# Performance work log

Measured on AMD Instinct MI355X. Metric: run time of the kernel, lower is better.

The kernel has to match this reference:

```python
import jax, jax.numpy as jnp
import numpy as np

INPUT_DIM = 1024
OUTPUT_DIM = 1024
NUM_HEADS = 16  # NOTE: torch .split(num_heads) => chunk SIZE = num_heads
N_CHUNKS = OUTPUT_DIM // NUM_HEADS  # 64 effective heads of dim 16
NEG_INF = -1e9


def setup_inputs() -> dict:
    key = jax.random.key(0)
    k1, k2, k3, k4 = jax.random.split(key, 4)
    B, S = 32, 256
    x = jax.random.normal(k1, (B, S, INPUT_DIM), dtype=jnp.float32)
    mask = jnp.ones((B, S), dtype=jnp.float32)
    # xavier-uniform-ish linear weights, torch layout [out, in]
    lim = float(np.sqrt(6.0 / (INPUT_DIM + OUTPUT_DIM)))
    Wq = jax.random.uniform(k2, (OUTPUT_DIM, INPUT_DIM), jnp.float32, -lim, lim)
    Wk = jax.random.uniform(k3, (OUTPUT_DIM, INPUT_DIM), jnp.float32, -lim, lim)
    Wv = jax.random.uniform(k4, (OUTPUT_DIM, INPUT_DIM), jnp.float32, -lim, lim)
    return {"batch_sequence": x, "sequence_mask": mask, "Wq": Wq, "Wk": Wk, "Wv": Wv}


def _split_heads(m):
    # [B,S,D] -> chunks of size NUM_HEADS stacked in dim 0: [C,B,S,H]
    B, S, D = m.shape
    return jnp.transpose(m.reshape(B, S, N_CHUNKS, NUM_HEADS), (2, 0, 1, 3))


def reference(batch_sequence, sequence_mask, Wq, Wk, Wv):
    q = _split_heads(batch_sequence @ Wq.T)  # [C,B,S,H]
    k = _split_heads(batch_sequence @ Wk.T)
    v = _split_heads(batch_sequence @ Wv.T)
    logits = jnp.einsum("cbqh,cbkh->cbqk", q, k) / jnp.sqrt(
        jnp.asarray(OUTPUT_DIM, batch_sequence.dtype)
    )
    mask2d = sequence_mask[:, :, None] * sequence_mask[:, None, :]  # [B,S,S]
    logits = jnp.where(mask2d[None] > 0, logits, NEG_INF)
    w = jax.nn.softmax(logits, axis=-1)
    out = jnp.einsum("cbqk,cbkh->cbqh", w, v)  # [C,B,S,H]
    B, S = batch_sequence.shape[:2]
    return jnp.transpose(out, (1, 2, 0, 3)).reshape(B, S, OUTPUT_DIM)
```

## Files before the change

### kernel.cpp

```cpp
#include <hip/hip_runtime.h>


typedef unsigned short u16;
typedef unsigned int u32;
typedef __attribute__((ext_vector_type(8))) short short8;
typedef __attribute__((ext_vector_type(4))) short short4v;
typedef __attribute__((ext_vector_type(4))) float floatx4;

#if __has_builtin(__builtin_amdgcn_mfma_f32_16x16x16bf16_1k)
#define MFMA16(A, B, C) __builtin_amdgcn_mfma_f32_16x16x16bf16_1k(A, B, C, 0, 0, 0)
#elif __has_builtin(__builtin_amdgcn_mfma_f32_16x16x16_bf16)
#define MFMA16(A, B, C) __builtin_amdgcn_mfma_f32_16x16x16_bf16(A, B, C, 0, 0, 0)
#else
__device__ __forceinline__ floatx4 mfma16_asm(short4v a, short4v b, floatx4 c) {
  floatx4 d;
  asm volatile("v_mfma_f32_16x16x16_bf16 %0, %1, %2, %3"
               : "=v"(d) : "v"(a), "v"(b), "v"(c));
  return d;
}
#define MFMA16(A, B, C) mfma16_asm(A, B, C)
#endif

#if __has_builtin(__builtin_amdgcn_exp2f)
#define EXP2(x) __builtin_amdgcn_exp2f(x)
#else
#define EXP2(x) __expf((x) * 0.6931471805599453f)
#endif

#define QSCALE 0.045084220f

__device__ __forceinline__ u16 f2bf(float f) {
  union { float f; u32 u; } x; x.f = f;
  u32 r = x.u + 0x7fffu + ((x.u >> 16) & 1u);
  return (u16)(r >> 16);
}
__device__ __forceinline__ float bf2f(u16 u) {
  union { u32 u; float f; } x; x.u = ((u32)u) << 16;
  return x.f;
}

__device__ __forceinline__ void gload16(const void* g, void* l) {
  typedef __attribute__((address_space(1))) const unsigned int gq;
  typedef __attribute__((address_space(3))) unsigned int lq;
  __builtin_amdgcn_global_load_lds((gq*)(size_t)g, (lq*)(size_t)l, 16, 0, 0);
}

#define GK 1024
#define QKS 20
#define VTS 264

__global__ __launch_bounds__(256) void cast_all(const float* __restrict__ x,
                                                const float* __restrict__ wq,
                                                const float* __restrict__ wk,
                                                const float* __restrict__ wv,
                                                u16* __restrict__ XB,
                                                u16* __restrict__ WB) {
  int bid = blockIdx.x;
  const float* src; u16* dst; int off;
  if (bid < 8192)       { src = x;  dst = XB;                 off = bid; }
  else if (bid < 9216)  { src = wq; dst = WB;                 off = bid - 8192; }
  else if (bid < 10240) { src = wk; dst = WB + 1024 * 1024;   off = bid - 9216; }
  else                  { src = wv; dst = WB + 2 * 1024 * 1024; off = bid - 10240; }
  int i = (off * 256 + threadIdx.x) * 4;
  float4 v = *(const float4*)(src + i);
  u32 lo = (u32)f2bf(v.x) | ((u32)f2bf(v.y) << 16);
  u32 hi = (u32)f2bf(v.z) | ((u32)f2bf(v.w) << 16);
  uint2 o; o.x = lo; o.y = hi;
  *(uint2*)(dst + i) = o;
}

template <bool MASKED>
__device__ __forceinline__ void attn_loop2(const u16* __restrict__ Ks,
                                           const u16* __restrict__ Vt,
                                           const short4v* bq, const float* mqv,
                                           const float* m_s,
                                           floatx4* oacc, floatx4* lacc,
                                           int col, int quad) {
  const short4v ones = {(short)0x3F80, (short)0x3F80, (short)0x3F80, (short)0x3F80};
#pragma unroll 4
  for (int kt = 0; kt < 16; kt++) {
    const int kb = kt * 16;
    short4v ak = *(const short4v*)(Ks + (kb + col) * QKS + quad * 4);
    short4v av = *(const short4v*)(Vt + col * VTS + kb + quad * 4);
    float mk[4];
    if (MASKED) {
#pragma unroll
      for (int i = 0; i < 4; i++) mk[i] = m_s[kb + quad * 4 + i];
    }
#pragma unroll
    for (int qt = 0; qt < 2; qt++) {
      floatx4 z = {0.f, 0.f, 0.f, 0.f};
      floatx4 st = MFMA16(ak, bq[qt], z);
      float e[4];
#pragma unroll
      for (int i = 0; i < 4; i++) {
        e[i] = EXP2(st[i]);
        if (MASKED) e[i] = (mqv[qt] * mk[i] > 0.f) ? e[i] : 0.f;
      }
      union { u32 u[2]; short4v s; } pk;
      pk.u[0] = __builtin_amdgcn_perm(__float_as_uint(e[1]), __float_as_uint(e[0]), 0x07060302u);
      pk.u[1] = __builtin_amdgcn_perm(__float_as_uint(e[3]), __float_as_uint(e[2]), 0x07060302u);
      lacc[qt] = MFMA16(ones, pk.s, lacc[qt]);
      oacc[qt] = MFMA16(av, pk.s, oacc[qt]);
    }
  }
}

__global__ __launch_bounds__(512, 4) void fused_qkv_attn(const u16* __restrict__ XB,
                                                         const u16* __restrict__ WB,
                                                         const float* __restrict__ mask,
                                                         float* __restrict__ out) {
  __shared__ __align__(16) u16 smem[22528];
  __shared__ float m_s[256];

  const int bid = blockIdx.x;
  const int b = bid & 31;
  const int c0 = (bid >> 5) * 2;
  const int t = threadIdx.x;
  const int wave = t >> 6;
  const int lane = t & 63;
  const int col = lane & 15;
  const int quad = lane >> 4;

  u16* const Xs = smem;
  u16* const Ws = smem + 16384;

  float mv = (t < 256) ? mask[b * 256 + t] : 1.0f;
  if (t < 256) m_s[t] = mv;
  const int allones = __syncthreads_and(mv > 0.f);

  const int r_loc = lane >> 3;
  const int sch = (lane & 7) ^ r_loc;

  const size_t xsrc = ((size_t)b * 256 + wave * 32 + r_loc) * GK + sch * 8;
  const int xdst = wave * 2048;

  const int gA = wave;
  const int ntA = gA >> 1;
  const size_t wsrcA =
      ((size_t)((ntA % 3) * 1024 + (c0 + ntA / 3) * 16 + (gA & 1) * 8 + r_loc)) * GK + sch * 8;
  size_t wsrcB = 0;
  const int gB = 8 + wave;
  if (wave < 4) {
    const int ntB = gB >> 1;
    wsrcB = ((size_t)((ntB % 3) * 1024 + (c0 + ntB / 3) * 16 + (gB & 1) * 8 + r_loc)) * GK + sch * 8;
  }

  floatx4 acc[2][6] = {};

  for (int k0 = 0; k0 < GK; k0 += 64) {
    __syncthreads();
#pragma unroll
    for (int g = 0; g < 4; g++)
      gload16(XB + xsrc + (size_t)g * 8 * GK + k0, Xs + xdst + g * 512);
    gload16(WB + wsrcA + k0, Ws + gA * 512);
    if (wave < 4) gload16(WB + wsrcB + k0, Ws + gB * 512);
    __syncthreads();
#pragma unroll
    for (int kk = 0; kk < 2; kk++) {
      const int pos = ((kk * 4 + quad) ^ (col & 7)) * 8;
      short8 af[2], bf[6];
#pragma unroll
      for (int mt = 0; mt < 2; mt++)
        af[mt] = *(const short8*)(Xs + (wave * 32 + mt * 16 + col) * 64 + pos);
#pragma unroll
      for (int nt = 0; nt < 6; nt++)
        bf[nt] = *(const short8*)(Ws + (nt * 16 + col) * 64 + pos);
#pragma unroll
      for (int mt = 0; mt < 2; mt++)
#pragma unroll
        for (int nt = 0; nt < 6; nt++)
          acc[mt][nt] = __builtin_amdgcn_mfma_f32_16x16x32_bf16(af[mt], bf[nt], acc[mt][nt], 0, 0, 0);
    }
  }

  u16* const Qs = smem;
  u16* const Ks = smem + 5120;
  u16* const Vt = smem + 10240;
  float* const l_s = (float*)(smem + 14464);
  float* const ot = (float*)smem;

#pragma unroll
  for (int h = 0; h < 2; h++) {
    __syncthreads();

#pragma unroll
    for (int mt = 0; mt < 2; mt++) {
      const int row = wave * 32 + mt * 16 + quad * 4;
#pragma unroll
      for (int r = 0; r < 4; r++) {
        Qs[(row + r) * QKS + col] = f2bf(acc[mt][3 * h + 0][r] * QSCALE);
        Ks[(row + r) * QKS + col] = f2bf(acc[mt][3 * h + 1][r]);
        Vt[col * VTS + row + r] = f2bf(acc[mt][3 * h + 2][r]);
      }
    }
    __syncthreads();

    const int q0 = wave * 32;
    short4v bq[2];
    float mqv[2];
#pragma unroll
    for (int qt = 0; qt < 2; qt++) {
      bq[qt] = *(const short4v*)(Qs + (q0 + qt * 16 + col) * QKS + quad * 4);
      mqv[qt] = m_s[q0 + qt * 16 + col];
    }

    floatx4 oacc[2] = {};
    floatx4 lacc[2] = {};
    if (allones)
      attn_loop2<false>(Ks, Vt, bq, mqv, m_s, oacc, lacc, col, quad);
    else
      attn_loop2<true>(Ks, Vt, bq, mqv, m_s, oacc, lacc, col, quad);

    __syncthreads();
#pragma unroll
    for (int qt = 0; qt < 2; qt++) {
      if (quad == 0) l_s[q0 + qt * 16 + col] = lacc[qt][0];
#pragma unroll
      for (int r = 0; r < 4; r++)
        ot[(quad * 4 + r) * 257 + q0 + qt * 16 + col] = oacc[qt][r];
    }
    __syncthreads();

    const int row = t >> 1;
    const int hb = (t & 1) * 8;
    float l = l_s[row];
    float* op = out + ((size_t)b * 256 + row) * 1024 + (c0 + h) * 16 + hb;
    float o[8];
    if (allones || l > 0.f) {
      float inv = 1.0f / l;
#pragma unroll
      for (int j = 0; j < 8; j++) o[j] = ot[(hb + j) * 257 + row] * inv;
    } else {
#pragma unroll
      for (int j = 0; j < 8; j++) o[j] = 0.f;
      for (int k = 0; k < 256; k++)
#pragma unroll
        for (int j = 0; j < 8; j++) o[j] += bf2f(Vt[(hb + j) * VTS + k]);
#pragma unroll
      for (int j = 0; j < 8; j++) o[j] *= (1.0f / 256.0f);
    }
#pragma unroll
    for (int g = 0; g < 2; g++) {
      float4 r;
      r.x = o[g * 4 + 0]; r.y = o[g * 4 + 1]; r.z = o[g * 4 + 2]; r.w = o[g * 4 + 3];
      *(float4*)(op + g * 4) = r;
    }
  }
}

extern "C" void kernel_launch(void* const* d_in, const int* in_sizes, int n_in,
                              void* d_out, int out_size, void* d_ws, size_t ws_size,
                              hipStream_t stream) {
  const float* x    = (const float*)d_in[0];
  const float* mask = (const float*)d_in[1];
  const float* Wq   = (const float*)d_in[2];
  const float* Wk   = (const float*)d_in[3];
  const float* Wv   = (const float*)d_in[4];
  float* out = (float*)d_out;

  u16* XB = (u16*)d_ws;
  u16* WB = XB + (size_t)8192 * 1024;

  cast_all<<<11264, 256, 0, stream>>>(x, Wq, Wk, Wv, XB, WB);
  fused_qkv_attn<<<1024, 512, 0, stream>>>(XB, WB, mask, out);
}
```

Baseline: 165.2 us.

## Double-buffer QKV projection GEMM with async global-to-LDS prefetch

Restructures the projection GEMM main loop to use two LDS buffers with a K-step of 32 instead of a single buffer with K-step 64. The next tile's global-to-LDS loads are issued before computing on the current tile, using explicit vmcnt waits and raw s_barrier in place of two __syncthreads per iteration. The aim is to overlap global memory latency with MFMA work. In exchange there are twice as many barrier steps, each doing half the MFMAs, plus reliance on a hand-tuned waitcnt scheme and a new swizzle layout.

```diff
diff --git a/kernel.cpp b/kernel.cpp
--- a/kernel.cpp
+++ b/kernel.cpp
@@ -122,57 +122,78 @@
   const int col = lane & 15;
   const int quad = lane >> 4;
 
-  u16* const Xs = smem;
-  u16* const Ws = smem + 16384;
+  u16* const Xs0 = smem;
+  u16* const Xs1 = smem + 8192;
+  u16* const Ws0 = smem + 16384;
+  u16* const Ws1 = smem + 19456;
 
   float mv = (t < 256) ? mask[b * 256 + t] : 1.0f;
   if (t < 256) m_s[t] = mv;
   const int allones = __syncthreads_and(mv > 0.f);
 
-  const int r_loc = lane >> 3;
-  const int sch = (lane & 7) ^ r_loc;
-
-  const size_t xsrc = ((size_t)b * 256 + wave * 32 + r_loc) * GK + sch * 8;
-  const int xdst = wave * 2048;
-
-  const int gA = wave;
-  const int ntA = gA >> 1;
-  const size_t wsrcA =
-      ((size_t)((ntA % 3) * 1024 + (c0 + ntA / 3) * 16 + (gA & 1) * 8 + r_loc)) * GK + sch * 8;
-  size_t wsrcB = 0;
-  const int gB = 8 + wave;
-  if (wave < 4) {
-    const int ntB = gB >> 1;
-    wsrcB = ((size_t)((ntB % 3) * 1024 + (c0 + ntB / 3) * 16 + (gB & 1) * 8 + r_loc)) * GK + sch * 8;
+  const int rl = lane >> 2;
+  const int ch = lane & 3;
+  const int sch = ch ^ ((rl >> 1) & 3);
+
+  const size_t xsrc = ((size_t)b * 256 + wave * 32 + rl) * GK + sch * 8;
+  const int xdst = wave * 1024;
+
+  size_t wsrc = 0;
+  if (wave < 6)
+    wsrc = ((size_t)((wave % 3) * 1024 + (c0 + wave / 3) * 16 + rl)) * GK + sch * 8;
+  const int wdst = wave * 512;
+
+  floatx4 acc[2][6] = {};
+
+  const int rpos = (quad ^ ((col >> 1) & 3)) * 8;
+  const int arow0 = (wave * 32 + col) * 32 + rpos;
+
+  gload16(XB + xsrc, Xs0 + xdst);
+  gload16(XB + xsrc + (size_t)16 * GK, Xs0 + xdst + 512);
+  if (wave < 6) gload16(WB + wsrc, Ws0 + wdst);
+
+  auto gemm_step = [&](int knext, const u16* Xc, const u16* Wc, u16* Xn, u16* Wn) {
+    if (knext >= 0) {
+      gload16(XB + xsrc + knext, Xn + xdst);
+      gload16(XB + xsrc + (size_t)16 * GK + knext, Xn + xdst + 512);
+      if (wave < 6) {
+        gload16(WB + wsrc + knext, Wn + wdst);
+        asm volatile("s_waitcnt vmcnt(3)" ::: "memory");
+      } else {
+        asm volatile("s_waitcnt vmcnt(2)" ::: "memory");
+      }
+    } else {
+      asm volatile("s_waitcnt vmcnt(0)" ::: "memory");
+    }
+    __builtin_amdgcn_sched_barrier(0);
+    __builtin_amdgcn_s_barrier();
+    __builtin_amdgcn_sched_barrier(0);
+
+    short8 af[2], bf[6];
+#pragma unroll
+    for (int mt = 0; mt < 2; mt++)
+      af[mt] = *(const short8*)(Xc + arow0 + mt * 512);
+#pragma unroll
+    for (int nt = 0; nt < 6; nt++)
+      bf[nt] = *(const short8*)(Wc + (nt * 16 + col) * 32 + rpos);
+#pragma unroll
+    for (int mt = 0; mt < 2; mt++)
+#pragma unroll
+      for (int nt = 0; nt < 6; nt++)
+        acc[mt][nt] = __builtin_amdgcn_mfma_f32_16x16x32_bf16(af[mt], bf[nt], acc[mt][nt], 0, 0, 0);
+
+    asm volatile("s_waitcnt lgkmcnt(0)" ::: "memory");
+    __builtin_amdgcn_sched_barrier(0);
+    __builtin_amdgcn_s_barrier();
+  };
+
+#pragma unroll 1
+  for (int tp = 0; tp < 15; tp++) {
+    gemm_step((2 * tp + 1) * 32, Xs0, Ws0, Xs1, Ws1);
+    gemm_step((2 * tp + 2) * 32, Xs1, Ws1, Xs0, Ws0);
   }
-
-  floatx4 acc[2][6] = {};
-
-  for (int k0 = 0; k0 < GK; k0 += 64) {
-    __syncthreads();
-#pragma unroll
-    for (int g = 0; g < 4; g++)
-      gload16(XB + xsrc + (size_t)g * 8 * GK + k0, Xs + xdst + g * 512);
-    gload16(WB + wsrcA + k0, Ws + gA * 512);
-    if (wave < 4) gload16(WB + wsrcB + k0, Ws + gB * 512);
-    __syncthreads();
-#pragma unroll
-    for (int kk = 0; kk < 2; kk++) {
-      const int pos = ((kk * 4 + quad) ^ (col & 7)) * 8;
-      short8 af[2], bf[6];
-#pragma unroll
-      for (int mt = 0; mt < 2; mt++)
-        af[mt] = *(const short8*)(Xs + (wave * 32 + mt * 16 + col) * 64 + pos);
-#pragma unroll
-      for (int nt = 0; nt < 6; nt++)
-        bf[nt] = *(const short8*)(Ws + (nt * 16 + col) * 64 + pos);
-#pragma unroll
-      for (int mt = 0; mt < 2; mt++)
-#pragma unroll
-        for (int nt = 0; nt < 6; nt++)
-          acc[mt][nt] = __builtin_amdgcn_mfma_f32_16x16x32_bf16(af[mt], bf[nt], acc[mt][nt], 0, 0, 0);
-    }
-  }
+  gemm_step(31 * 32, Xs0, Ws0, Xs1, Ws1);
+  gemm_step(-1, Xs1, Ws1, Xs0, Ws0);
 
   u16* const Qs = smem;
   u16* const Ks = smem + 5120;
```

New measurement: 167.5 us. No clear change (+1.4%).

## Fuse activation bf16 cast into QKV GEMM with double-buffered weight loads

Applied to the files above, without the earlier changes.

Removes the separate pass that casts x to bf16 in a workspace. The attention kernel now loads fp32 x directly into registers, converts it with packed bf16 conversion instructions, and writes it to LDS. Weight tiles are double-buffered in LDS so the next tile's global loads overlap the current MFMA step. This saves writing and rereading the 16MB bf16 copy of x, but each of the 32 blocks per batch row now reads and converts that row's fp32 x (twice the bytes of the bf16 copy), and LDS use per block rises.

```diff
diff --git a/kernel.cpp b/kernel.cpp
--- a/kernel.cpp
+++ b/kernel.cpp
@@ -39,6 +39,12 @@
   return x.f;
 }
 
+__device__ __forceinline__ u32 pkbf(float lo, float hi) {
+  u32 d;
+  asm("v_cvt_pk_bf16_f32 %0, %1, %2" : "=v"(d) : "v"(lo), "v"(hi));
+  return d;
+}
+
 __device__ __forceinline__ void gload16(const void* g, void* l) {
   typedef __attribute__((address_space(1))) const unsigned int gq;
   typedef __attribute__((address_space(3))) unsigned int lq;
@@ -49,24 +55,19 @@
 #define QKS 20
 #define VTS 264
 
-__global__ __launch_bounds__(256) void cast_all(const float* __restrict__ x,
-                                                const float* __restrict__ wq,
-                                                const float* __restrict__ wk,
-                                                const float* __restrict__ wv,
-                                                u16* __restrict__ XB,
-                                                u16* __restrict__ WB) {
+__global__ __launch_bounds__(256) void cast_w(const float* __restrict__ wq,
+                                              const float* __restrict__ wk,
+                                              const float* __restrict__ wv,
+                                              u16* __restrict__ WB) {
   int bid = blockIdx.x;
-  const float* src; u16* dst; int off;
-  if (bid < 8192)       { src = x;  dst = XB;                 off = bid; }
-  else if (bid < 9216)  { src = wq; dst = WB;                 off = bid - 8192; }
-  else if (bid < 10240) { src = wk; dst = WB + 1024 * 1024;   off = bid - 9216; }
-  else                  { src = wv; dst = WB + 2 * 1024 * 1024; off = bid - 10240; }
-  int i = (off * 256 + threadIdx.x) * 4;
+  const float* src = (bid < 1024) ? wq : (bid < 2048) ? wk : wv;
+  int seg = bid >> 10;
+  int i = ((bid & 1023) * 256 + threadIdx.x) * 4;
   float4 v = *(const float4*)(src + i);
-  u32 lo = (u32)f2bf(v.x) | ((u32)f2bf(v.y) << 16);
-  u32 hi = (u32)f2bf(v.z) | ((u32)f2bf(v.w) << 16);
-  uint2 o; o.x = lo; o.y = hi;
-  *(uint2*)(dst + i) = o;
+  uint2 o;
+  o.x = pkbf(v.x, v.y);
+  o.y = pkbf(v.z, v.w);
+  *(uint2*)(WB + (size_t)seg * 1024 * 1024 + i) = o;
 }
 
 template <bool MASKED>
@@ -106,11 +107,11 @@
   }
 }
 
-__global__ __launch_bounds__(512, 4) void fused_qkv_attn(const u16* __restrict__ XB,
+__global__ __launch_bounds__(512, 4) void fused_qkv_attn(const float* __restrict__ x,
                                                          const u16* __restrict__ WB,
                                                          const float* __restrict__ mask,
                                                          float* __restrict__ out) {
-  __shared__ __align__(16) u16 smem[22528];
+  __shared__ __align__(16) u16 smem[28672];
   __shared__ float m_s[256];
 
   const int bid = blockIdx.x;
@@ -123,39 +124,69 @@
   const int quad = lane >> 4;
 
   u16* const Xs = smem;
-  u16* const Ws = smem + 16384;
+  u16* const WsA = smem + 16384;
+  u16* const WsB = smem + 22528;
 
   float mv = (t < 256) ? mask[b * 256 + t] : 1.0f;
   if (t < 256) m_s[t] = mv;
   const int allones = __syncthreads_and(mv > 0.f);
 
-  const int r_loc = lane >> 3;
-  const int sch = (lane & 7) ^ r_loc;
-
-  const size_t xsrc = ((size_t)b * 256 + wave * 32 + r_loc) * GK + sch * 8;
-  const int xdst = wave * 2048;
-
+  const float* const xg = x + ((size_t)b * 256 + (t >> 3)) * GK + (t & 7) * 8;
+  const int wbase = (t >> 3) * 64 + (((t & 7) ^ ((t >> 3) & 7)) * 8);
+
+  const int r_loc8 = lane >> 3;
+  const int sch8 = (lane & 7) ^ r_loc8;
   const int gA = wave;
   const int ntA = gA >> 1;
   const size_t wsrcA =
-      ((size_t)((ntA % 3) * 1024 + (c0 + ntA / 3) * 16 + (gA & 1) * 8 + r_loc)) * GK + sch * 8;
+      ((size_t)((ntA % 3) * 1024 + (c0 + ntA / 3) * 16 + (gA & 1) * 8 + r_loc8)) * GK + sch8 * 8;
   size_t wsrcB = 0;
   const int gB = 8 + wave;
   if (wave < 4) {
     const int ntB = gB >> 1;
-    wsrcB = ((size_t)((ntB % 3) * 1024 + (c0 + ntB / 3) * 16 + (gB & 1) * 8 + r_loc)) * GK + sch * 8;
+    wsrcB = ((size_t)((ntB % 3) * 1024 + (c0 + ntB / 3) * 16 + (gB & 1) * 8 + r_loc8)) * GK + sch8 * 8;
   }
 
   floatx4 acc[2][6] = {};
-
-  for (int k0 = 0; k0 < GK; k0 += 64) {
-    __syncthreads();
-#pragma unroll
-    for (int g = 0; g < 4; g++)
-      gload16(XB + xsrc + (size_t)g * 8 * GK + k0, Xs + xdst + g * 512);
-    gload16(WB + wsrcA + k0, Ws + gA * 512);
-    if (wave < 4) gload16(WB + wsrcB + k0, Ws + gB * 512);
-    __syncthreads();
+  float4 xv[8];
+
+  gload16(WB + wsrcA, WsA + gA * 512);
+  if (wave < 4) gload16(WB + wsrcB, WsA + gB * 512);
+#pragma unroll
+  for (int p = 0; p < 4; p++) {
+#pragma unroll
+    for (int q = 0; q < 2; q++)
+      xv[p * 2 + q] = *(const float4*)(xg + p * 65536 + q * 4);
+  }
+  asm volatile("s_waitcnt vmcnt(0)" ::: "memory");
+#pragma unroll
+  for (int p = 0; p < 4; p++) {
+    uint4 w;
+    w.x = pkbf(xv[p * 2].x, xv[p * 2].y);
+    w.y = pkbf(xv[p * 2].z, xv[p * 2].w);
+    w.z = pkbf(xv[p * 2 + 1].x, xv[p * 2 + 1].y);
+    w.w = pkbf(xv[p * 2 + 1].z, xv[p * 2 + 1].w);
+    *(uint4*)(Xs + wbase + p * 4096) = w;
+  }
+  asm volatile("s_waitcnt lgkmcnt(0)" ::: "memory");
+  __builtin_amdgcn_sched_barrier(0);
+
+  auto gemm_step = [&](int tnext, const u16* Wc, u16* Wn) {
+    __builtin_amdgcn_s_barrier();
+    __builtin_amdgcn_sched_barrier(0);
+
+    if (tnext >= 0) {
+      const int k0n = tnext * 64;
+      gload16(WB + wsrcA + k0n, Wn + gA * 512);
+      if (wave < 4) gload16(WB + wsrcB + k0n, Wn + gB * 512);
+#pragma unroll
+      for (int p = 0; p < 4; p++) {
+#pragma unroll
+        for (int q = 0; q < 2; q++)
+          xv[p * 2 + q] = *(const float4*)(xg + k0n + p * 65536 + q * 4);
+      }
+    }
+
 #pragma unroll
     for (int kk = 0; kk < 2; kk++) {
       const int pos = ((kk * 4 + quad) ^ (col & 7)) * 8;
@@ -165,13 +196,39 @@
         af[mt] = *(const short8*)(Xs + (wave * 32 + mt * 16 + col) * 64 + pos);
 #pragma unroll
       for (int nt = 0; nt < 6; nt++)
-        bf[nt] = *(const short8*)(Ws + (nt * 16 + col) * 64 + pos);
+        bf[nt] = *(const short8*)(Wc + (nt * 16 + col) * 64 + pos);
 #pragma unroll
       for (int mt = 0; mt < 2; mt++)
 #pragma unroll
         for (int nt = 0; nt < 6; nt++)
           acc[mt][nt] = __builtin_amdgcn_mfma_f32_16x16x32_bf16(af[mt], bf[nt], acc[mt][nt], 0, 0, 0);
     }
+
+    asm volatile("s_waitcnt lgkmcnt(0)" ::: "memory");
+    __builtin_amdgcn_sched_barrier(0);
+    __builtin_amdgcn_s_barrier();
+    __builtin_amdgcn_sched_barrier(0);
+
+    if (tnext >= 0) {
+      asm volatile("s_waitcnt vmcnt(0)" ::: "memory");
+#pragma unroll
+      for (int p = 0; p < 4; p++) {
+        uint4 w;
+        w.x = pkbf(xv[p * 2].x, xv[p * 2].y);
+        w.y = pkbf(xv[p * 2].z, xv[p * 2].w);
+        w.z = pkbf(xv[p * 2 + 1].x, xv[p * 2 + 1].y);
+        w.w = pkbf(xv[p * 2 + 1].z, xv[p * 2 + 1].w);
+        *(uint4*)(Xs + wbase + p * 4096) = w;
+      }
+      asm volatile("s_waitcnt lgkmcnt(0)" ::: "memory");
+      __builtin_amdgcn_sched_barrier(0);
+    }
+  };
+
+#pragma unroll 1
+  for (int tp = 0; tp < 8; tp++) {
+    gemm_step(2 * tp + 1, WsA, WsB);
+    gemm_step((tp == 7) ? -1 : 2 * tp + 2, WsB, WsA);
   }
 
   u16* const Qs = smem;
@@ -259,9 +316,8 @@
   const float* Wv   = (const float*)d_in[4];
   float* out = (float*)d_out;
 
-  u16* XB = (u16*)d_ws;
-  u16* WB = XB + (size_t)8192 * 1024;
-
-  cast_all<<<11264, 256, 0, stream>>>(x, Wq, Wk, Wv, XB, WB);
-  fused_qkv_attn<<<1024, 512, 0, stream>>>(XB, WB, mask, out);
-}
+  u16* WB = (u16*)d_ws;
+
+  cast_w<<<3072, 256, 0, stream>>>(Wq, Wk, Wv, WB);
+  fused_qkv_attn<<<1024, 512, 0, stream>>>(x, WB, mask, out);
+}
```

New measurement: 190.3 us. 15.2% more time.

## Double-buffer X tiles and register-stage W loads in the fused QKV GEMM loop

Applied to the files above, without the earlier changes.

The QKV projection loop now double-buffers the X tile in shared memory. The next K-slice is issued while the current one is consumed, and W is prefetched into registers and written to LDS at the start of each step, so global load latency overlaps the MFMA work. Explicit waitcnt, sched_barrier and s_barrier calls replace the two __syncthreads per iteration. It also raises wave priority around the attention MFMA/exp block. LDS grows from about 45KB to about 78KB per block, which may reduce occupancy below the 4 blocks requested by the launch bounds.

```diff
diff --git a/kernel.cpp b/kernel.cpp
--- a/kernel.cpp
+++ b/kernel.cpp
@@ -89,6 +89,7 @@
     }
 #pragma unroll
     for (int qt = 0; qt < 2; qt++) {
+      __builtin_amdgcn_s_setprio(1);
       floatx4 z = {0.f, 0.f, 0.f, 0.f};
       floatx4 st = MFMA16(ak, bq[qt], z);
       float e[4];
@@ -102,6 +103,7 @@
       pk.u[1] = __builtin_amdgcn_perm(__float_as_uint(e[3]), __float_as_uint(e[2]), 0x07060302u);
       lacc[qt] = MFMA16(ones, pk.s, lacc[qt]);
       oacc[qt] = MFMA16(av, pk.s, oacc[qt]);
+      __builtin_amdgcn_s_setprio(0);
     }
   }
 }
@@ -110,7 +112,7 @@
                                                          const u16* __restrict__ WB,
                                                          const float* __restrict__ mask,
                                                          float* __restrict__ out) {
-  __shared__ __align__(16) u16 smem[22528];
+  __shared__ __align__(16) u16 smem[38912];
   __shared__ float m_s[256];
 
   const int bid = blockIdx.x;
@@ -122,8 +124,9 @@
   const int col = lane & 15;
   const int quad = lane >> 4;
 
-  u16* const Xs = smem;
-  u16* const Ws = smem + 16384;
+  u16* const Xs0 = smem;
+  u16* const Xs1 = smem + 16384;
+  u16* const Ws  = smem + 32768;
 
   float mv = (t < 256) ? mask[b * 256 + t] : 1.0f;
   if (t < 256) m_s[t] = mv;
@@ -145,24 +148,45 @@
     const int ntB = gB >> 1;
     wsrcB = ((size_t)((ntB % 3) * 1024 + (c0 + ntB / 3) * 16 + (gB & 1) * 8 + r_loc)) * GK + sch * 8;
   }
+  u16* const wdA = Ws + gA * 512 + lane * 8;
+  u16* const wdB = Ws + gB * 512 + lane * 8;
 
   floatx4 acc[2][6] = {};
 
-  for (int k0 = 0; k0 < GK; k0 += 64) {
-    __syncthreads();
-#pragma unroll
-    for (int g = 0; g < 4; g++)
-      gload16(XB + xsrc + (size_t)g * 8 * GK + k0, Xs + xdst + g * 512);
-    gload16(WB + wsrcA + k0, Ws + gA * 512);
-    if (wave < 4) gload16(WB + wsrcB + k0, Ws + gB * 512);
-    __syncthreads();
+#pragma unroll
+  for (int g = 0; g < 4; g++)
+    gload16(XB + xsrc + (size_t)g * 8 * GK, Xs0 + xdst + g * 512);
+  __builtin_amdgcn_sched_barrier(0);
+  uint4 wA = *(const uint4*)(WB + wsrcA);
+  uint4 wB = {};
+  if (wave < 4) wB = *(const uint4*)(WB + wsrcB);
+
+  auto gemm_step = [&](int k0n, const u16* Xc, u16* Xn) {
+    asm volatile("s_waitcnt vmcnt(0)" ::: "memory");
+    __builtin_amdgcn_sched_barrier(0);
+    *(uint4*)wdA = wA;
+    if (wave < 4) *(uint4*)wdB = wB;
+    __builtin_amdgcn_sched_barrier(0);
+    if (k0n >= 0) {
+#pragma unroll
+      for (int g = 0; g < 4; g++)
+        gload16(XB + xsrc + (size_t)g * 8 * GK + k0n, Xn + xdst + g * 512);
+      wA = *(const uint4*)(WB + wsrcA + k0n);
+      if (wave < 4) wB = *(const uint4*)(WB + wsrcB + k0n);
+    }
+    __builtin_amdgcn_sched_barrier(0);
+    asm volatile("s_waitcnt lgkmcnt(0)" ::: "memory");
+    __builtin_amdgcn_sched_barrier(0);
+    __builtin_amdgcn_s_barrier();
+    __builtin_amdgcn_sched_barrier(0);
+
 #pragma unroll
     for (int kk = 0; kk < 2; kk++) {
       const int pos = ((kk * 4 + quad) ^ (col & 7)) * 8;
       short8 af[2], bf[6];
 #pragma unroll
       for (int mt = 0; mt < 2; mt++)
-        af[mt] = *(const short8*)(Xs + (wave * 32 + mt * 16 + col) * 64 + pos);
+        af[mt] = *(const short8*)(Xc + (wave * 32 + mt * 16 + col) * 64 + pos);
 #pragma unroll
       for (int nt = 0; nt < 6; nt++)
         bf[nt] = *(const short8*)(Ws + (nt * 16 + col) * 64 + pos);
@@ -172,6 +196,17 @@
         for (int nt = 0; nt < 6; nt++)
           acc[mt][nt] = __builtin_amdgcn_mfma_f32_16x16x32_bf16(af[mt], bf[nt], acc[mt][nt], 0, 0, 0);
     }
+
+    asm volatile("s_waitcnt lgkmcnt(0)" ::: "memory");
+    __builtin_amdgcn_sched_barrier(0);
+    __builtin_amdgcn_s_barrier();
+    __builtin_amdgcn_sched_barrier(0);
+  };
+
+#pragma unroll 1
+  for (int tp = 0; tp < 8; tp++) {
+    gemm_step((2 * tp + 1) * 64, Xs0, Xs1);
+    gemm_step((tp == 7) ? -1 : (2 * tp + 2) * 64, Xs1, Xs0);
   }
 
   u16* const Qs = smem;
```

After: 167.8 us. About the same (+1.6%).
